# Kernel tuning notes

Measured on AMD Instinct MI355X. Metric: run time of the kernel, lower is better.

The kernel has to match this reference:

```python
import jax, jax.numpy as jnp
import numpy as np

B, T, H = 4096, 2048, 5


def setup_inputs() -> dict:
    key = jax.random.key(0)
    ks = jax.random.split(key, 10)
    s = 1.0 / np.sqrt(H)  # PyTorch RNN/Linear init scale (uniform(-s, s)); use normal for test data
    return {
        "hidden": jax.random.normal(ks[0], (1, B, H), dtype=jnp.float32),
        "X": jax.random.normal(ks[1], (B, T, 1), dtype=jnp.float32),
        "W_ih": jax.random.normal(ks[2], (H, 1), dtype=jnp.float32) * s,
        "W_hh": jax.random.normal(ks[3], (H, H), dtype=jnp.float32) * s,
        "b_ih": jax.random.normal(ks[4], (H,), dtype=jnp.float32) * s,
        "b_hh": jax.random.normal(ks[5], (H,), dtype=jnp.float32) * s,
        "fc1_w": jax.random.normal(ks[6], (H, H), dtype=jnp.float32) * s,
        "fc1_b": jax.random.normal(ks[7], (H,), dtype=jnp.float32) * s,
        "fc2_w": jax.random.normal(ks[8], (1, H), dtype=jnp.float32) * s,
        "fc2_b": jax.random.normal(ks[9], (1,), dtype=jnp.float32) * s,
    }


def reference(hidden, X, W_ih, W_hh, b_ih, b_hh, fc1_w, fc1_b, fc2_w, fc2_b):
    # Single-layer tanh RNN, batch_first. Precompute input projection once:
    # x_proj: [T, B, H]
    x_proj = jnp.einsum("bti,hi->tbh", X, W_ih) + b_ih + b_hh
    h0 = hidden[0]  # [B, H]

    def step(h, xp_t):
        h_new = jnp.tanh(xp_t + h @ W_hh.T)
        return h_new, h_new

    h_last, outs = jax.lax.scan(step, h0, x_proj)  # outs: [T, B, H]
    outs = jnp.transpose(outs, (1, 0, 2))  # [B, T, H]
    hid = jax.nn.relu(outs @ fc1_w.T + fc1_b)  # [B, T, 5]
    y = hid @ fc2_w.T + fc2_b  # [B, T, 1]
    return y
```

## Files before the change

kernel.cpp:

```cpp
#include <hip/hip_runtime.h>
#include <math.h>


#define B_ 4096
#define T_ 2048

#define DPPF(v, ctrl) __int_as_float(__builtin_amdgcn_update_dpp(0, __float_as_int(v), (ctrl), 0xF, 0xF, true))
#define QP_X1 0xB1
#define QP_X2 0x4E
#define QP_X3 0x1B
#define RHM   0x141

__device__ __forceinline__ float precise_tanh(float x) {
    const float L_hi = 1.44269504f;
    const float L_lo = 1.9259630e-8f;
    const float LN2  = 0.69314718f;

    float xc = fminf(fmaxf(x, -15.0f), 15.0f);
    float y2 = xc + xc;
    float a  = y2 * L_hi;
    float dl = fmaf(y2, L_hi, -a);
    dl = fmaf(y2, L_lo, dl);
    float e0 = __builtin_amdgcn_exp2f(a);
    float e  = fmaf(e0, dl * LN2, e0);
    float d  = e + 1.0f;
    float r0 = __builtin_amdgcn_rcpf(d);
    float r  = fmaf(fmaf(-d, r0, 1.0f), r0, r0);
    return fmaf(-2.0f, r, 1.0f);
}

#define EXCHANGE(rr, hh)                                   \
    do {                                                   \
        rr[0] = (hh);                                      \
        rr[1] = DPPF((hh), QP_X1);                         \
        rr[2] = DPPF((hh), QP_X2);                         \
        rr[3] = DPPF((hh), QP_X3);                         \
        rr[7] = DPPF((hh), RHM);                           \
        rr[6] = DPPF(rr[7], QP_X1);                        \
        rr[5] = DPPF(rr[7], QP_X2);                        \
        rr[4] = DPPF(rr[7], QP_X3);                        \
    } while (0)

__global__ __launch_bounds__(64, 1) void wavernn_kernel(
    const float* __restrict__ hidden, const float* __restrict__ X,
    const float* __restrict__ W_ih, const float* __restrict__ W_hh,
    const float* __restrict__ b_ih, const float* __restrict__ b_hh,
    const float* __restrict__ fc1_w, const float* __restrict__ fc1_b,
    const float* __restrict__ fc2_w, const float* __restrict__ fc2_b,
    float* __restrict__ out)
{
    const int lane = threadIdx.x;
    const int j = lane & 7;
    const int grp = (blockIdx.x * 64 + lane) >> 3;

    float w[8], f[8];
#pragma unroll
    for (int k = 0; k < 8; ++k) {
        const int c = j ^ k;
        const bool live = (j < 5) && (c < 5);
        w[k] = live ? W_hh[j * 5 + c] : 0.0f;
        f[k] = live ? fc1_w[j * 5 + c] : 0.0f;
    }
    const float wih  = (j < 5) ? W_ih[j] : 0.0f;
    const float bias = (j < 5) ? (b_ih[j] + b_hh[j]) : 0.0f;
    const float fb   = (j < 5) ? fc1_b[j] : 0.0f;
    const float w2   = (j < 5) ? fc2_w[j] : 0.0f;
    const float b2   = fc2_b[0];

    float h = (j < 5) ? hidden[grp * 5 + j] : 0.0f;

    float r[8];
    EXCHANGE(r, h);

    const float* __restrict__ xrow = X  + (size_t)grp * T_;
    float*       __restrict__ yrow = out + (size_t)grp * T_;

    for (int t = 0; t < T_; t += 4) {
        const float4 x4 = *reinterpret_cast<const float4*>(xrow + t);
        float y0, y1, y2, y3;
#pragma unroll
        for (int u = 0; u < 4; ++u) {
            const float x = (u == 0) ? x4.x : (u == 1) ? x4.y : (u == 2) ? x4.z : x4.w;

            float acc = fmaf(x, wih, bias);
            acc = fmaf(w[0], r[0], acc); acc = fmaf(w[1], r[1], acc);
            acc = fmaf(w[2], r[2], acc); acc = fmaf(w[3], r[3], acc);
            acc = fmaf(w[4], r[4], acc); acc = fmaf(w[5], r[5], acc);
            acc = fmaf(w[6], r[6], acc); acc = fmaf(w[7], r[7], acc);
            h = precise_tanh(acc);

            EXCHANGE(r, h);

            float g = fb;
            g = fmaf(f[0], r[0], g); g = fmaf(f[1], r[1], g);
            g = fmaf(f[2], r[2], g); g = fmaf(f[3], r[3], g);
            g = fmaf(f[4], r[4], g); g = fmaf(f[5], r[5], g);
            g = fmaf(f[6], r[6], g); g = fmaf(f[7], r[7], g);
            const float hid = fmaxf(g, 0.0f);

            float p = hid * w2;
            p += DPPF(p, QP_X1);
            p += DPPF(p, QP_X2);
            p += DPPF(p, RHM);
            const float y = p + b2;
            if (u == 0) y0 = y; else if (u == 1) y1 = y; else if (u == 2) y2 = y; else y3 = y;
        }
        if (j == 0) {
            *reinterpret_cast<float4*>(yrow + t) = make_float4(y0, y1, y2, y3);
        }
    }
}

extern "C" void kernel_launch(void* const* d_in, const int* in_sizes, int n_in,
                              void* d_out, int out_size, void* d_ws, size_t ws_size,
                              hipStream_t stream)
{
    const float* hidden = (const float*)d_in[0];
    const float* X      = (const float*)d_in[1];
    const float* W_ih   = (const float*)d_in[2];
    const float* W_hh   = (const float*)d_in[3];
    const float* b_ih   = (const float*)d_in[4];
    const float* b_hh   = (const float*)d_in[5];
    const float* fc1_w  = (const float*)d_in[6];
    const float* fc1_b  = (const float*)d_in[7];
    const float* fc2_w  = (const float*)d_in[8];
    const float* fc2_b  = (const float*)d_in[9];
    float* out = (float*)d_out;

    wavernn_kernel<<<dim3(B_ * 8 / 64), dim3(64), 0, stream>>>(
        hidden, X, W_ih, W_hh, b_ih, b_hh, fc1_w, fc1_b, fc2_w, fc2_b, out);
}
```

Before: 352.1 us.

## Split RNN recurrence and FC head into two kernels via workspace buffer

Splits the fused kernel into two. The first runs only the serial tanh recurrence and writes every hidden state to a workspace buffer as float4 chunks. The second is a fully parallel kernel that reads those states and computes fc1+relu+fc2. The aim is to shorten the serial critical path by taking the FC math and DPP reductions out of the recurrence loop. In exchange it writes and re-reads about 256MB of intermediate hidden states, and it falls back to the fused kernel if the workspace is too small.

```diff
diff --git a/kernel.cpp b/kernel.cpp
--- a/kernel.cpp
+++ b/kernel.cpp
@@ -15,7 +15,6 @@
     const float L_hi = 1.44269504f;
     const float L_lo = 1.9259630e-8f;
     const float LN2  = 0.69314718f;
-
     float xc = fminf(fmaxf(x, -15.0f), 15.0f);
     float y2 = xc + xc;
     float a  = y2 * L_hi;
@@ -41,7 +40,104 @@
         rr[4] = DPPF(rr[7], QP_X3);                        \
     } while (0)
 
-__global__ __launch_bounds__(64, 1) void wavernn_kernel(
+__global__ __launch_bounds__(64, 1) void rnn_phase1(
+    const float* __restrict__ hidden, const float* __restrict__ X,
+    const float* __restrict__ W_ih, const float* __restrict__ W_hh,
+    const float* __restrict__ b_ih, const float* __restrict__ b_hh,
+    float4* __restrict__ hbuf)
+{
+    const int lane = threadIdx.x;
+    const int j = lane & 7;
+    const int grp = (blockIdx.x * 64 + lane) >> 3;
+
+    float w[8];
+#pragma unroll
+    for (int k = 0; k < 8; ++k) {
+        const int c = j ^ k;
+        const bool live = (j < 5) && (c < 5);
+        w[k] = live ? W_hh[j * 5 + c] : 0.0f;
+    }
+    const float wih  = (j < 5) ? W_ih[j] : 0.0f;
+    const float bias = (j < 5) ? (b_ih[j] + b_hh[j]) : 0.0f;
+
+    float h = (j < 5) ? hidden[grp * 5 + j] : 0.0f;
+    float r[8];
+    EXCHANGE(r, h);
+
+    const float* __restrict__ xrow = X + (size_t)grp * T_;
+    float4*      __restrict__ hout = hbuf + ((size_t)grp * (T_ / 4)) * 8 + j;
+
+    for (int t = 0; t < T_; t += 4) {
+        const float4 x4 = *reinterpret_cast<const float4*>(xrow + t);
+        float4 hs;
+#pragma unroll
+        for (int u = 0; u < 4; ++u) {
+            const float x = (u == 0) ? x4.x : (u == 1) ? x4.y : (u == 2) ? x4.z : x4.w;
+            float acc = fmaf(x, wih, bias);
+            acc = fmaf(w[0], r[0], acc); acc = fmaf(w[1], r[1], acc);
+            acc = fmaf(w[2], r[2], acc); acc = fmaf(w[3], r[3], acc);
+            acc = fmaf(w[4], r[4], acc); acc = fmaf(w[5], r[5], acc);
+            acc = fmaf(w[6], r[6], acc); acc = fmaf(w[7], r[7], acc);
+            h = precise_tanh(acc);
+            EXCHANGE(r, h);
+            if (u == 0) hs.x = h; else if (u == 1) hs.y = h;
+            else if (u == 2) hs.z = h; else hs.w = h;
+        }
+        hout[(t >> 2) * 8] = hs;
+    }
+}
+
+__global__ __launch_bounds__(256) void fc_phase2(
+    const float4* __restrict__ hbuf,
+    const float* __restrict__ fc1_w, const float* __restrict__ fc1_b,
+    const float* __restrict__ fc2_w, const float* __restrict__ fc2_b,
+    float* __restrict__ out)
+{
+    const int g = blockIdx.x * 256 + threadIdx.x;
+    const int b  = g >> 9;
+    const int tq = g & 511;
+
+    float f1[5][5], fb[5], w2[5];
+#pragma unroll
+    for (int i = 0; i < 5; ++i) {
+#pragma unroll
+        for (int c = 0; c < 5; ++c) f1[i][c] = fc1_w[i * 5 + c];
+        fb[i] = fc1_b[i];
+        w2[i] = fc2_w[i];
+    }
+    const float b2 = fc2_b[0];
+
+    const float4* src = hbuf + (size_t)g * 8;
+    float4 v[5];
+#pragma unroll
+    for (int c = 0; c < 5; ++c) v[c] = src[c];
+
+    float4 y4;
+#pragma unroll
+    for (int u = 0; u < 4; ++u) {
+        const float h0 = (u==0)?v[0].x:(u==1)?v[0].y:(u==2)?v[0].z:v[0].w;
+        const float h1 = (u==0)?v[1].x:(u==1)?v[1].y:(u==2)?v[1].z:v[1].w;
+        const float h2 = (u==0)?v[2].x:(u==1)?v[2].y:(u==2)?v[2].z:v[2].w;
+        const float h3 = (u==0)?v[3].x:(u==1)?v[3].y:(u==2)?v[3].z:v[3].w;
+        const float h4 = (u==0)?v[4].x:(u==1)?v[4].y:(u==2)?v[4].z:v[4].w;
+        float y = b2;
+#pragma unroll
+        for (int i = 0; i < 5; ++i) {
+            float gacc = fb[i];
+            gacc = fmaf(f1[i][0], h0, gacc);
+            gacc = fmaf(f1[i][1], h1, gacc);
+            gacc = fmaf(f1[i][2], h2, gacc);
+            gacc = fmaf(f1[i][3], h3, gacc);
+            gacc = fmaf(f1[i][4], h4, gacc);
+            y = fmaf(w2[i], fmaxf(gacc, 0.0f), y);
+        }
+        if (u == 0) y4.x = y; else if (u == 1) y4.y = y;
+        else if (u == 2) y4.z = y; else y4.w = y;
+    }
+    *reinterpret_cast<float4*>(out + (size_t)b * T_ + 4 * tq) = y4;
+}
+
+__global__ __launch_bounds__(64, 1) void wavernn_fused(
     const float* __restrict__ hidden, const float* __restrict__ X,
     const float* __restrict__ W_ih, const float* __restrict__ W_hh,
     const float* __restrict__ b_ih, const float* __restrict__ b_hh,
@@ -68,7 +164,6 @@
     const float b2   = fc2_b[0];
 
     float h = (j < 5) ? hidden[grp * 5 + j] : 0.0f;
-
     float r[8];
     EXCHANGE(r, h);
 
@@ -81,23 +176,19 @@
 #pragma unroll
         for (int u = 0; u < 4; ++u) {
             const float x = (u == 0) ? x4.x : (u == 1) ? x4.y : (u == 2) ? x4.z : x4.w;
-
             float acc = fmaf(x, wih, bias);
             acc = fmaf(w[0], r[0], acc); acc = fmaf(w[1], r[1], acc);
             acc = fmaf(w[2], r[2], acc); acc = fmaf(w[3], r[3], acc);
             acc = fmaf(w[4], r[4], acc); acc = fmaf(w[5], r[5], acc);
             acc = fmaf(w[6], r[6], acc); acc = fmaf(w[7], r[7], acc);
             h = precise_tanh(acc);
-
             EXCHANGE(r, h);
-
             float g = fb;
             g = fmaf(f[0], r[0], g); g = fmaf(f[1], r[1], g);
             g = fmaf(f[2], r[2], g); g = fmaf(f[3], r[3], g);
             g = fmaf(f[4], r[4], g); g = fmaf(f[5], r[5], g);
             g = fmaf(f[6], r[6], g); g = fmaf(f[7], r[7], g);
             const float hid = fmaxf(g, 0.0f);
-
             float p = hid * w2;
             p += DPPF(p, QP_X1);
             p += DPPF(p, QP_X2);
@@ -127,6 +218,15 @@
     const float* fc2_b  = (const float*)d_in[9];
     float* out = (float*)d_out;
 
-    wavernn_kernel<<<dim3(B_ * 8 / 64), dim3(64), 0, stream>>>(
-        hidden, X, W_ih, W_hh, b_ih, b_hh, fc1_w, fc1_b, fc2_w, fc2_b, out);
-}
+    const size_t need = (size_t)B_ * T_ * 8 * sizeof(float);
+    if (ws_size >= need) {
+        float4* hbuf = (float4*)d_ws;
+        rnn_phase1<<<dim3(B_ * 8 / 64), dim3(64), 0, stream>>>(
+            hidden, X, W_ih, W_hh, b_ih, b_hh, hbuf);
+        fc_phase2<<<dim3(B_ * T_ / 4 / 256), dim3(256), 0, stream>>>(
+            hbuf, fc1_w, fc1_b, fc2_w, fc2_b, out);
+    } else {
+        wavernn_fused<<<dim3(B_ * 8 / 64), dim3(64), 0, stream>>>(
+            hidden, X, W_ih, W_hh, b_ih, b_hh, fc1_w, fc1_b, fc2_w, fc2_b, out);
+    }
+}
```

Measured after the change: 375.9 us. +6.8%, slower.
